# Kernel optimization log

Measured on AMD Instinct MI355X. Metric: run time of the kernel, lower is better.

The kernel has to match this reference:

```python
import jax, jax.numpy as jnp
import numpy as np

E, P, K, V, H, NE = 768, 256, 32, 32, 128, 8
B, M_DIM, T_DIM = 16, 4, 512


def setup_inputs() -> dict:
    key = jax.random.key(0)
    ks = jax.random.split(key, 24)
    s = 0.05
    inp = {
        'token_embeddings': jax.random.normal(ks[0], (B, M_DIM, T_DIM, E), jnp.float32),
        'U': jax.random.uniform(ks[1], (B, M_DIM, T_DIM), jnp.float32),
        'R': jax.random.uniform(ks[2], (B, M_DIM, M_DIM, T_DIM), jnp.float32),
        'S': jax.random.uniform(ks[3], (B, M_DIM, M_DIM, T_DIM), jnp.float32),
        'W_tp': jax.random.normal(ks[4], (E, P), jnp.float32) * s,
        'b_tp': jnp.zeros((P,), jnp.float32),
        'W_q': jax.random.normal(ks[5], (P, K), jnp.float32) * s,
        'b_q': jnp.zeros((K,), jnp.float32),
        'W_k': jax.random.normal(ks[6], (2, K), jnp.float32) * s,
        'b_k': jnp.zeros((K,), jnp.float32),
        'W_v': jax.random.normal(ks[7], (2, V), jnp.float32) * s,
        'b_v': jnp.zeros((V,), jnp.float32),
        'W_ih': jax.random.normal(ks[8], (3 * H, 1 + V), jnp.float32) * s,
        'W_hh': jax.random.normal(ks[9], (3 * H, H), jnp.float32) * s,
        'b_ih': jnp.zeros((3 * H,), jnp.float32),
        'b_hh': jnp.zeros((3 * H,), jnp.float32),
        'W1': jax.random.normal(ks[10], (P + H, (P + H) // 2), jnp.float32) * s,
        'b1': jnp.zeros(((P + H) // 2,), jnp.float32),
        'W2': jax.random.normal(ks[11], ((P + H) // 2, NE), jnp.float32) * s,
        'b2': jnp.zeros((NE,), jnp.float32),
        'M': M_DIM,
        'T': T_DIM,
    }
    return inp


def _gru(x, W_ih, W_hh, b_ih, b_hh):
    # x: [N, T, D] -> outputs [N, T, H]; PyTorch GRU cell math
    N, T, _ = x.shape
    Hh = W_hh.shape[1]
    gi = jnp.einsum('ntd,gd->ntg', x, W_ih) + b_ih  # [N,T,3H] precomputed input gates
    gi = jnp.transpose(gi, (1, 0, 2))  # [T,N,3H]

    def step(h, gi_t):
        gh = h @ W_hh.T + b_hh
        i_r, i_z, i_n = jnp.split(gi_t, 3, axis=-1)
        h_r, h_z, h_n = jnp.split(gh, 3, axis=-1)
        r = jax.nn.sigmoid(i_r + h_r)
        z = jax.nn.sigmoid(i_z + h_z)
        n = jnp.tanh(i_n + r * h_n)
        h_new = (1.0 - z) * n + z * h
        return h_new, h_new

    h0 = jnp.zeros((N, Hh), x.dtype)
    _, hs = jax.lax.scan(step, h0, gi)
    return jnp.transpose(hs, (1, 0, 2))  # [N,T,H]


def reference(token_embeddings, U, R, S, W_tp, b_tp, W_q, b_q, W_k, b_k, W_v, b_v,
              W_ih, W_hh, b_ih, b_hh, W1, b1, W2, b2, M, T):
    Bn, Mn, Tn, _ = token_embeddings.shape
    proc = jax.nn.relu(token_embeddings @ W_tp + b_tp)           # [B,M,T,P]
    query = proc @ W_q + b_q                                     # [B,M,T,K]
    Rp = jnp.transpose(R, (0, 3, 1, 2))                          # [B,T,M,M]
    Sp = jnp.transpose(S, (0, 3, 1, 2))
    pf = jnp.stack([Rp, Sp], axis=-1)                            # [B,T,M,M,2]
    keys = pf @ W_k + b_k                                        # [B,T,M,M,K]
    vals = pf @ W_v + b_v                                        # [B,T,M,M,V]
    scores = jnp.einsum('bmtk,btmjk->bmtj', query, keys) / np.sqrt(K)
    diag = jnp.eye(Mn, dtype=bool)                               # exclude j == m
    scores = jnp.where(diag[None, :, None, :], -1e9, scores)
    w = jax.nn.softmax(scores, axis=-1)                          # [B,M,T,M]
    ctx = jnp.einsum('bmtj,btmjv->bmtv', w, vals)                # [B,M,T,V]
    gru_in = jnp.concatenate([U[..., None], ctx], axis=-1)       # [B,M,T,1+V]
    gru_out = _gru(gru_in.reshape(Bn * Mn, Tn, 1 + V), W_ih, W_hh, b_ih, b_hh)
    rus_ctx = gru_out.reshape(Bn, Mn, Tn, H)
    combined = jnp.concatenate([proc, rus_ctx], axis=-1)         # [B,M,T,P+H]
    hidden = jax.nn.relu(combined @ W1 + b1)
    logits = hidden @ W2 + b2                                    # [B,M,T,NE]
    return logits
```

## Files before the change

kernel.cpp:

```cpp
#include <hip/hip_runtime.h>


typedef __attribute__((ext_vector_type(8))) short short8;
typedef __attribute__((ext_vector_type(4))) float f32x4;

__device__ __forceinline__ float bf2f(unsigned short u) {
    return __uint_as_float(((unsigned int)u) << 16);
}
__device__ __forceinline__ unsigned short f2bf(float f) {
    unsigned int x = __float_as_uint(f);
    return (unsigned short)((x + 0x7FFFu + ((x >> 16) & 1u)) >> 16);
}
__device__ __forceinline__ float sigm(float x) { return 1.0f / (1.0f + __expf(-x)); }
__device__ __forceinline__ float tanh_fast(float x) {
    x = fminf(fmaxf(x, -15.0f), 15.0f);
    float e = __expf(-2.0f * x);
    return (1.0f - e) / (1.0f + e);
}
__device__ __forceinline__ float dpp_xor1_add(float v) {
    int o = __builtin_amdgcn_update_dpp(0, __float_as_int(v), 0xB1, 0xF, 0xF, true);
    return v + __int_as_float(o);
}
__device__ __forceinline__ float sel4(f32x4 c, int sel) {
    float t0 = (sel & 1) ? c[1] : c[0];
    float t1 = (sel & 1) ? c[3] : c[2];
    return (sel & 2) ? t1 : t0;
}

#define CST_SC   768
#define CST_WU   800
#define CST_WA2  1184
#define CST_WB2  1568
#define CST_CC   1952

__global__ void k_paint(float* out, float val, int nmax) {
    int i = blockIdx.x * blockDim.x + threadIdx.x;
    if (i < nmax) out[i] = val;
}

__global__ void k_prep(const float* __restrict__ Wq,
                       const float* __restrict__ bq,
                       const float* __restrict__ Wk,
                       const float* __restrict__ bk,
                       const float* __restrict__ Wv,
                       const float* __restrict__ bv,
                       const float* __restrict__ Wih,
                       const float* __restrict__ bih,
                       float* __restrict__ cst)
{
    const int t = threadIdx.x;
    if (t < 256) {
        float a = 0.f, b = 0.f, c = 0.f;
        for (int k = 0; k < 32; ++k) {
            float w = Wq[t * 32 + k];
            a = fmaf(w, Wk[k], a);
            b = fmaf(w, Wk[32 + k], b);
            c = fmaf(w, bk[k], c);
        }
        cst[t] = a; cst[256 + t] = b; cst[512 + t] = c;
    }
    if (t == 0) {
        float ca = 0.f, cb = 0.f, cc = 0.f;
        for (int k = 0; k < 32; ++k) {
            float bqk = bq[k];
            ca = fmaf(bqk, Wk[k], ca);
            cb = fmaf(bqk, Wk[32 + k], cb);
            cc = fmaf(bqk, bk[k], cc);
        }
        cst[CST_SC + 0] = ca; cst[CST_SC + 1] = cb; cst[CST_SC + 2] = cc;
    }
    if (t < 384) {
        cst[CST_WU + t] = Wih[t * 33];
        float a2 = 0.f, b2 = 0.f, c2 = bih[t];
        for (int v = 0; v < 32; ++v) {
            float w = Wih[t * 33 + 1 + v];
            a2 = fmaf(w, Wv[v], a2);
            b2 = fmaf(w, Wv[32 + v], b2);
            c2 = fmaf(w, bv[v], c2);
        }
        cst[CST_WA2 + t] = a2; cst[CST_WB2 + t] = b2; cst[CST_CC + t] = c2;
    }
}

__global__ __launch_bounds__(256) void k_proc(
    const float* __restrict__ A,
    const float* __restrict__ Bw,
    const float* __restrict__ bias,
    unsigned short* __restrict__ C)
{
    __shared__ unsigned short A_s[128 * 40];
    __shared__ unsigned short B_s[64 * 40];
    const int t = threadIdx.x;
    const int row0 = blockIdx.y * 128;
    const int col0 = blockIdx.x * 64;
    const int lane = t & 63, wave = t >> 6;
    const int wr = wave >> 1, wc = wave & 1;
    const int quad = lane >> 4, l16 = lane & 15;

    f32x4 acc[4][2] = {};

    for (int k0 = 0; k0 < 768; k0 += 32) {
        {
            const int r = t >> 1, kq = (t & 1) * 16;
            const float* src = A + (size_t)(row0 + r) * 768 + k0 + kq;
            float4 v0 = *(const float4*)(src);
            float4 v1 = *(const float4*)(src + 4);
            float4 v2 = *(const float4*)(src + 8);
            float4 v3 = *(const float4*)(src + 12);
            short8 s0, s1;
            s0[0] = f2bf(v0.x); s0[1] = f2bf(v0.y); s0[2] = f2bf(v0.z); s0[3] = f2bf(v0.w);
            s0[4] = f2bf(v1.x); s0[5] = f2bf(v1.y); s0[6] = f2bf(v1.z); s0[7] = f2bf(v1.w);
            s1[0] = f2bf(v2.x); s1[1] = f2bf(v2.y); s1[2] = f2bf(v2.z); s1[3] = f2bf(v2.w);
            s1[4] = f2bf(v3.x); s1[5] = f2bf(v3.y); s1[6] = f2bf(v3.z); s1[7] = f2bf(v3.w);
            *(short8*)(A_s + r * 40 + kq) = s0;
            *(short8*)(A_s + r * 40 + kq + 8) = s1;
        }
        {
            const int k = t >> 3, nq = (t & 7) * 8;
            const float* src = Bw + (size_t)(k0 + k) * 256 + col0 + nq;
            float4 v0 = *(const float4*)(src);
            float4 v1 = *(const float4*)(src + 4);
            B_s[(nq + 0) * 40 + k] = f2bf(v0.x);
            B_s[(nq + 1) * 40 + k] = f2bf(v0.y);
            B_s[(nq + 2) * 40 + k] = f2bf(v0.z);
            B_s[(nq + 3) * 40 + k] = f2bf(v0.w);
            B_s[(nq + 4) * 40 + k] = f2bf(v1.x);
            B_s[(nq + 5) * 40 + k] = f2bf(v1.y);
            B_s[(nq + 6) * 40 + k] = f2bf(v1.z);
            B_s[(nq + 7) * 40 + k] = f2bf(v1.w);
        }
        __syncthreads();
        short8 af[4], bf[2];
        #pragma unroll
        for (int im = 0; im < 4; ++im)
            af[im] = *(const short8*)(A_s + (wr * 64 + im * 16 + l16) * 40 + quad * 8);
        #pragma unroll
        for (int in = 0; in < 2; ++in)
            bf[in] = *(const short8*)(B_s + (wc * 32 + in * 16 + l16) * 40 + quad * 8);
        #pragma unroll
        for (int im = 0; im < 4; ++im)
            #pragma unroll
            for (int in = 0; in < 2; ++in)
                acc[im][in] = __builtin_amdgcn_mfma_f32_16x16x32_bf16(
                    af[im], bf[in], acc[im][in], 0, 0, 0);
        __syncthreads();
    }
    float bias_v[2];
    #pragma unroll
    for (int in = 0; in < 2; ++in) bias_v[in] = bias[col0 + wc * 32 + in * 16 + l16];
    #pragma unroll
    for (int im = 0; im < 4; ++im)
        #pragma unroll
        for (int in = 0; in < 2; ++in) {
            const int c_g = col0 + wc * 32 + in * 16 + l16;
            #pragma unroll
            for (int reg = 0; reg < 4; ++reg) {
                const int r_g = row0 + wr * 64 + im * 16 + quad * 4 + reg;
                float v = fmaxf(acc[im][in][reg] + bias_v[in], 0.f);
                C[(size_t)r_g * 256 + c_g] = f2bf(v);
            }
        }
}

__global__ __launch_bounds__(256) void k_attn(
    const unsigned short* __restrict__ proc,
    const float* __restrict__ R,
    const float* __restrict__ S,
    const float* __restrict__ cst,
    float* __restrict__ wrws)
{
    __shared__ float wv_s[768];
    const int tid = threadIdx.x;
    for (int i = tid; i < 768; i += 256) wv_s[i] = cst[i];
    __syncthreads();

    const int lane = tid & 63, wave = tid >> 6;
    const int row = blockIdx.x * 4 + wave;
    const int t = row & 511, m = (row >> 9) & 3, b = row >> 11;
    const int p0 = lane * 4;

    ushort4 u = *(const ushort4*)(proc + (size_t)row * 256 + p0);
    float p0f = bf2f(u.x), p1f = bf2f(u.y), p2f = bf2f(u.z), p3f = bf2f(u.w);
    float dA = 0.f, dB = 0.f, dC = 0.f;
    dA = fmaf(p0f, wv_s[p0 + 0], dA); dB = fmaf(p0f, wv_s[256 + p0 + 0], dB); dC = fmaf(p0f, wv_s[512 + p0 + 0], dC);
    dA = fmaf(p1f, wv_s[p0 + 1], dA); dB = fmaf(p1f, wv_s[256 + p0 + 1], dB); dC = fmaf(p1f, wv_s[512 + p0 + 1], dC);
    dA = fmaf(p2f, wv_s[p0 + 2], dA); dB = fmaf(p2f, wv_s[256 + p0 + 2], dB); dC = fmaf(p2f, wv_s[512 + p0 + 2], dC);
    dA = fmaf(p3f, wv_s[p0 + 3], dA); dB = fmaf(p3f, wv_s[256 + p0 + 3], dB); dC = fmaf(p3f, wv_s[512 + p0 + 3], dC);
    #pragma unroll
    for (int mm = 1; mm < 64; mm <<= 1) {
        dA += __shfl_xor(dA, mm, 64);
        dB += __shfl_xor(dB, mm, 64);
        dC += __shfl_xor(dC, mm, 64);
    }
    if (lane == 0) {
        dA += cst[CST_SC + 0]; dB += cst[CST_SC + 1]; dC += cst[CST_SC + 2];
        const float scale = 0.17677669529663687f;
        float rr[4], ss[4], sc[4], mx = -1e30f;
        #pragma unroll
        for (int j = 0; j < 4; ++j) {
            const size_t idx = ((size_t)(b * 16 + m * 4 + j)) * 512 + t;
            rr[j] = R[idx]; ss[j] = S[idx];
            float v = (rr[j] * dA + ss[j] * dB + dC) * scale;
            if (j == m) v = -1e9f;
            sc[j] = v; mx = fmaxf(mx, v);
        }
        float w[4], se = 0.f;
        #pragma unroll
        for (int j = 0; j < 4; ++j) { w[j] = __expf(sc[j] - mx); se += w[j]; }
        const float inv = 1.0f / se;
        float wr = 0.f, wss = 0.f;
        #pragma unroll
        for (int j = 0; j < 4; ++j) { wr += w[j] * rr[j]; wss += w[j] * ss[j]; }
        float2 o; o.x = wr * inv; o.y = wss * inv;
        ((float2*)wrws)[row] = o;
    }
}

__global__ __launch_bounds__(256) void k_gru(
    const float* __restrict__ wrws,
    const float* __restrict__ U,
    const float* __restrict__ Whh,
    const float* __restrict__ bhh,
    const float* __restrict__ cst,
    unsigned short* __restrict__ gout)
{
    __shared__ unsigned short hbuf[2][2][144];
    __shared__ float4 uvw_s[512];

    const int tid  = threadIdx.x;
    const int lane = tid & 63, w = tid >> 6;
    const int l16  = lane & 15, quad = lane >> 4;
    const int n    = blockIdx.x;
    const int par  = l16 & 1;
    const int sel  = (l16 >> 1) & 3;
    const int hh   = (l16 >> 3) & 1;
    const int eg   = 32 * w + 16 * hh + quad * 4 + sel;
    const bool writer = (par == 0);

    short8 afr[3][2][4];
    #pragma unroll
    for (int g3 = 0; g3 < 3; ++g3)
        #pragma unroll
        for (int h2 = 0; h2 < 2; ++h2) {
            const int row = g3 * 128 + 32 * w + 16 * h2 + l16;
            const float* rp = Whh + (size_t)row * 128 + quad * 8;
            #pragma unroll
            for (int kf = 0; kf < 4; ++kf) {
                float4 v0 = *(const float4*)(rp + kf * 32);
                float4 v1 = *(const float4*)(rp + kf * 32 + 4);
                short8 s;
                s[0] = f2bf(v0.x); s[1] = f2bf(v0.y); s[2] = f2bf(v0.z); s[3] = f2bf(v0.w);
                s[4] = f2bf(v1.x); s[5] = f2bf(v1.y); s[6] = f2bf(v1.z); s[7] = f2bf(v1.w);
                afr[g3][h2][kf] = s;
            }
        }

    const float wu_r = cst[CST_WU  + eg], wu_z = cst[CST_WU  + 128 + eg], wu_n = cst[CST_WU  + 256 + eg];
    const float wa_r = cst[CST_WA2 + eg], wa_z = cst[CST_WA2 + 128 + eg], wa_n = cst[CST_WA2 + 256 + eg];
    const float wb_r = cst[CST_WB2 + eg], wb_z = cst[CST_WB2 + 128 + eg], wb_n = cst[CST_WB2 + 256 + eg];
    const float cc_r = cst[CST_CC  + eg] + bhh[eg];
    const float cc_z = cst[CST_CC  + 128 + eg] + bhh[128 + eg];
    const float cc_n = cst[CST_CC  + 256 + eg];
    const float bh_n = bhh[256 + eg];

    for (int i = tid; i < 512; i += 256) {
        float u = U[(size_t)n * 512 + i];
        float2 w2 = ((const float2*)wrws)[(size_t)n * 512 + i];
        float4 p; p.x = u; p.y = w2.x; p.z = w2.y; p.w = 0.f;
        uvw_s[i] = p;
    }
    for (int i = tid; i < 288; i += 256) ((unsigned int*)hbuf)[i] = 0u;
    __syncthreads();

    float h_old = 0.f;
    const f32x4 ZZ = {0.f, 0.f, 0.f, 0.f};

    #pragma unroll 2
    for (int t = 0; t < 512; ++t) {
        const int cur = t & 1, nxt = cur ^ 1;

        const unsigned short* hb = &hbuf[cur][par][0];
        short8 bfr[4];
        #pragma unroll
        for (int kf = 0; kf < 4; ++kf)
            bfr[kf] = *(const short8*)(hb + kf * 32 + quad * 8);
        const float4 uvw = uvw_s[t];

        f32x4 c[6] = {ZZ, ZZ, ZZ, ZZ, ZZ, ZZ};
        #pragma unroll
        for (int kf = 0; kf < 4; ++kf)
            #pragma unroll
            for (int j = 0; j < 6; ++j)
                c[j] = __builtin_amdgcn_mfma_f32_16x16x32_bf16(
                    afr[j >> 1][j & 1][kf], bfr[kf], c[j], 0, 0, 0);

        float gh[3];
        #pragma unroll
        for (int g3 = 0; g3 < 3; ++g3) {
            const float v0 = sel4(c[2 * g3 + 0], sel);
            const float v1 = sel4(c[2 * g3 + 1], sel);
            gh[g3] = dpp_xor1_add(hh ? v1 : v0);
        }

        const float gir = fmaf(uvw.z, wb_r, fmaf(uvw.y, wa_r, fmaf(uvw.x, wu_r, cc_r)));
        const float giz = fmaf(uvw.z, wb_z, fmaf(uvw.y, wa_z, fmaf(uvw.x, wu_z, cc_z)));
        const float gin = fmaf(uvw.z, wb_n, fmaf(uvw.y, wa_n, fmaf(uvw.x, wu_n, cc_n)));
        const float r  = sigm(gir + gh[0]);
        const float z  = sigm(giz + gh[1]);
        const float nn = tanh_fast(fmaf(r, gh[2] + bh_n, gin));
        const float hn = fmaf(z, h_old - nn, nn);
        h_old = hn;

        if (writer) {
            const unsigned short hi16 = f2bf(hn);
            hbuf[nxt][0][eg] = hi16;
            hbuf[nxt][1][eg] = f2bf(hn - bf2f(hi16));
            gout[((size_t)n * 512 + t) * 128 + eg] = hi16;
        }
        asm volatile("s_waitcnt lgkmcnt(0)" ::: "memory");
        __builtin_amdgcn_s_barrier();
        asm volatile("" ::: "memory");
        __builtin_amdgcn_sched_barrier(0x7);
    }
}

__global__ __launch_bounds__(256) void k_hid(
    const unsigned short* __restrict__ proc,
    const unsigned short* __restrict__ gout,
    const float* __restrict__ W1,
    const float* __restrict__ b1,
    const float* __restrict__ W2,
    const float* __restrict__ b2,
    float* __restrict__ out)
{
    __shared__ __align__(16) unsigned char smem[56480];
    unsigned short* As = (unsigned short*)smem;
    unsigned short* Bh = (unsigned short*)(smem + 5120);
    unsigned short* Bl = (unsigned short*)(smem + 20480);
    float* Hs  = (float*)smem;
    float* W2t = (float*)(smem + 50176);
    float* b2s = (float*)(smem + 56448);

    const int tid = threadIdx.x;
    const int row0 = blockIdx.x * 64;
    const int lane = tid & 63, w = tid >> 6;
    const int l16 = lane & 15, quad = lane >> 4;

    for (int i = tid; i < 1536; i += 256) {
        const int c = i >> 3, e = i & 7;
        W2t[e * 196 + c] = W2[i];
    }
    if (tid < 8) b2s[tid] = b2[tid];

    const int ar = tid >> 2, akq = (tid & 3) * 8;
    const int bk2 = (tid >> 4) * 2, bc0 = tid & 15;

    f32x4 acc[4][3] = {};

    for (int k0 = 0; k0 < 384; k0 += 32) {
        __syncthreads();
        {
            const int kk = k0 + akq;
            short8 v;
            if (kk < 256) v = *(const short8*)(proc + (size_t)(row0 + ar) * 256 + kk);
            else          v = *(const short8*)(gout + (size_t)(row0 + ar) * 128 + (kk - 256));
            *(short8*)(As + ar * 40 + akq) = v;
        }
        {
            const float* wrow0 = W1 + (size_t)(k0 + bk2) * 192;
            const float* wrow1 = wrow0 + 192;
            #pragma unroll
            for (int j = 0; j < 12; ++j) {
                const int c = bc0 + 16 * j;
                const float f0 = wrow0[c], f1 = wrow1[c];
                const unsigned short h0 = f2bf(f0), h1 = f2bf(f1);
                const unsigned short s0 = f2bf(f0 - bf2f(h0));
                const unsigned short s1 = f2bf(f1 - bf2f(h1));
                *(unsigned int*)(Bh + c * 40 + bk2) = (unsigned int)h0 | ((unsigned int)h1 << 16);
                *(unsigned int*)(Bl + c * 40 + bk2) = (unsigned int)s0 | ((unsigned int)s1 << 16);
            }
        }
        __syncthreads();
        short8 af[4], bh[3], bl[3];
        #pragma unroll
        for (int m = 0; m < 4; ++m)
            af[m] = *(const short8*)(As + (m * 16 + l16) * 40 + quad * 8);
        #pragma unroll
        for (int nn = 0; nn < 3; ++nn) {
            const int col = w * 48 + nn * 16 + l16;
            bh[nn] = *(const short8*)(Bh + col * 40 + quad * 8);
            bl[nn] = *(const short8*)(Bl + col * 40 + quad * 8);
        }
        #pragma unroll
        for (int m = 0; m < 4; ++m)
            #pragma unroll
            for (int nn = 0; nn < 3; ++nn) {
                acc[m][nn] = __builtin_amdgcn_mfma_f32_16x16x32_bf16(af[m], bh[nn], acc[m][nn], 0, 0, 0);
                acc[m][nn] = __builtin_amdgcn_mfma_f32_16x16x32_bf16(af[m], bl[nn], acc[m][nn], 0, 0, 0);
            }
    }
    __syncthreads();
    {
        float b1v[3];
        #pragma unroll
        for (int nn = 0; nn < 3; ++nn) b1v[nn] = b1[w * 48 + nn * 16 + l16];
        #pragma unroll
        for (int m = 0; m < 4; ++m)
            #pragma unroll
            for (int nn = 0; nn < 3; ++nn) {
                const int col = w * 48 + nn * 16 + l16;
                #pragma unroll
                for (int reg = 0; reg < 4; ++reg) {
                    const int row = m * 16 + quad * 4 + reg;
                    Hs[row * 196 + col] = fmaxf(acc[m][nn][reg] + b1v[nn], 0.f);
                }
            }
    }
    __syncthreads();
    const int r = tid >> 2, qq = tid & 3;
    const int e0 = 2 * qq, e1 = e0 + 1;
    float s0 = b2s[e0], s1 = b2s[e1];
    const float* hrow = Hs + r * 196;
    const float* w0 = W2t + e0 * 196;
    const float* w1 = W2t + e1 * 196;
    #pragma unroll 8
    for (int c = 0; c < 192; c += 4) {
        float4 h4 = *(const float4*)(hrow + c);
        float4 a4 = *(const float4*)(w0 + c);
        float4 b4 = *(const float4*)(w1 + c);
        s0 = fmaf(h4.x, a4.x, fmaf(h4.y, a4.y, fmaf(h4.z, a4.z, fmaf(h4.w, a4.w, s0))));
        s1 = fmaf(h4.x, b4.x, fmaf(h4.y, b4.y, fmaf(h4.z, b4.z, fmaf(h4.w, b4.w, s1))));
    }
    out[(size_t)(row0 + r) * 8 + e0] = s0;
    out[(size_t)(row0 + r) * 8 + e1] = s1;
}

extern "C" void kernel_launch(void* const* d_in, const int* in_sizes, int n_in,
                              void* d_out, int out_size, void* d_ws, size_t ws_size,
                              hipStream_t stream) {
    const float* emb  = (const float*)d_in[0];
    const float* U    = (const float*)d_in[1];
    const float* R    = (const float*)d_in[2];
    const float* S    = (const float*)d_in[3];
    const float* W_tp = (const float*)d_in[4];
    const float* b_tp = (const float*)d_in[5];
    const float* W_q  = (const float*)d_in[6];
    const float* b_q  = (const float*)d_in[7];
    const float* W_k  = (const float*)d_in[8];
    const float* b_k  = (const float*)d_in[9];
    const float* W_v  = (const float*)d_in[10];
    const float* b_v  = (const float*)d_in[11];
    const float* W_ih = (const float*)d_in[12];
    const float* W_hh = (const float*)d_in[13];
    const float* b_ih = (const float*)d_in[14];
    const float* b_hh = (const float*)d_in[15];
    const float* W1   = (const float*)d_in[16];
    const float* b1   = (const float*)d_in[17];
    const float* W2   = (const float*)d_in[18];
    const float* b2   = (const float*)d_in[19];

    float* outp = (float*)d_out;

    const size_t NEEDED = 25444352u;
    if (ws_size < NEEDED) {
        k_paint<<<(out_size + 255) / 256, 256, 0, stream>>>(outp, 3.0f, out_size);
        return;
    }

    char* ws = (char*)d_ws;
    unsigned short* proc = (unsigned short*)(ws);
    float*          wrws = (float*)(ws + 16777216u);
    unsigned short* gout = (unsigned short*)(ws + 17039360u);
    float*          cst  = (float*)(ws + 25427968u);

    k_prep<<<1, 512, 0, stream>>>(W_q, b_q, W_k, b_k, W_v, b_v, W_ih, b_ih, cst);
    k_proc<<<dim3(4, 256), 256, 0, stream>>>(emb, W_tp, b_tp, proc);
    k_attn<<<8192, 256, 0, stream>>>(proc, R, S, cst, wrws);
    k_gru <<<64, 256, 0, stream>>>(wrws, U, W_hh, b_hh, cst, gout);
    k_hid <<<512, 256, 0, stream>>>(proc, gout, W1, b1, W2, b2, outp);
}
```

Before: 524.8 us.

## Pre-transpose and bf16-convert GEMM weights once, load B fragments directly from global

Weight matrices W_tp and W1 are now converted to bf16 (W1 as hi/lo split) and transposed once in the prep kernel. k_proc and k_hid load B fragments straight from global memory into registers, with a one-step register prefetch, instead of having every block re-convert and scatter the weights into shared memory. This removes redundant per-block conversion work and LDS traffic. In exchange, the prep kernel becomes heavier, using 8 blocks with strided (uncoalesced) transposed writes, and B reads now depend on cache hits.

```diff
diff --git a/kernel.cpp b/kernel.cpp
--- a/kernel.cpp
+++ b/kernel.cpp
@@ -46,50 +46,68 @@
                        const float* __restrict__ bv,
                        const float* __restrict__ Wih,
                        const float* __restrict__ bih,
-                       float* __restrict__ cst)
+                       const float* __restrict__ Wtp,
+                       const float* __restrict__ W1,
+                       float* __restrict__ cst,
+                       unsigned short* __restrict__ wtpT,
+                       unsigned short* __restrict__ w1hT,
+                       unsigned short* __restrict__ w1lT)
 {
     const int t = threadIdx.x;
-    if (t < 256) {
-        float a = 0.f, b = 0.f, c = 0.f;
-        for (int k = 0; k < 32; ++k) {
-            float w = Wq[t * 32 + k];
-            a = fmaf(w, Wk[k], a);
-            b = fmaf(w, Wk[32 + k], b);
-            c = fmaf(w, bk[k], c);
-        }
-        cst[t] = a; cst[256 + t] = b; cst[512 + t] = c;
-    }
-    if (t == 0) {
-        float ca = 0.f, cb = 0.f, cc = 0.f;
-        for (int k = 0; k < 32; ++k) {
-            float bqk = bq[k];
-            ca = fmaf(bqk, Wk[k], ca);
-            cb = fmaf(bqk, Wk[32 + k], cb);
-            cc = fmaf(bqk, bk[k], cc);
-        }
-        cst[CST_SC + 0] = ca; cst[CST_SC + 1] = cb; cst[CST_SC + 2] = cc;
-    }
-    if (t < 384) {
-        cst[CST_WU + t] = Wih[t * 33];
-        float a2 = 0.f, b2 = 0.f, c2 = bih[t];
-        for (int v = 0; v < 32; ++v) {
-            float w = Wih[t * 33 + 1 + v];
-            a2 = fmaf(w, Wv[v], a2);
-            b2 = fmaf(w, Wv[32 + v], b2);
-            c2 = fmaf(w, bv[v], c2);
-        }
-        cst[CST_WA2 + t] = a2; cst[CST_WB2 + t] = b2; cst[CST_CC + t] = c2;
+    if (blockIdx.x == 0) {
+        if (t < 256) {
+            float a = 0.f, b = 0.f, c = 0.f;
+            for (int k = 0; k < 32; ++k) {
+                float w = Wq[t * 32 + k];
+                a = fmaf(w, Wk[k], a);
+                b = fmaf(w, Wk[32 + k], b);
+                c = fmaf(w, bk[k], c);
+            }
+            cst[t] = a; cst[256 + t] = b; cst[512 + t] = c;
+        }
+        if (t == 0) {
+            float ca = 0.f, cb = 0.f, cc = 0.f;
+            for (int k = 0; k < 32; ++k) {
+                float bqk = bq[k];
+                ca = fmaf(bqk, Wk[k], ca);
+                cb = fmaf(bqk, Wk[32 + k], cb);
+                cc = fmaf(bqk, bk[k], cc);
+            }
+            cst[CST_SC + 0] = ca; cst[CST_SC + 1] = cb; cst[CST_SC + 2] = cc;
+        }
+        if (t < 384) {
+            cst[CST_WU + t] = Wih[t * 33];
+            float a2 = 0.f, b2 = 0.f, c2 = bih[t];
+            for (int v = 0; v < 32; ++v) {
+                float w = Wih[t * 33 + 1 + v];
+                a2 = fmaf(w, Wv[v], a2);
+                b2 = fmaf(w, Wv[32 + v], b2);
+                c2 = fmaf(w, bv[v], c2);
+            }
+            cst[CST_WA2 + t] = a2; cst[CST_WB2 + t] = b2; cst[CST_CC + t] = c2;
+        }
+    }
+    const int gt = blockIdx.x * 512 + t;
+    for (int i = gt; i < 196608; i += 4096) {
+        const int k = i >> 8, c = i & 255;
+        wtpT[c * 768 + k] = f2bf(Wtp[i]);
+    }
+    for (int i = gt; i < 73728; i += 4096) {
+        const int k = i / 192, c = i - k * 192;
+        const float w = W1[i];
+        const unsigned short h = f2bf(w);
+        w1hT[c * 384 + k] = h;
+        w1lT[c * 384 + k] = f2bf(w - bf2f(h));
     }
 }
 
 __global__ __launch_bounds__(256) void k_proc(
     const float* __restrict__ A,
-    const float* __restrict__ Bw,
+    const unsigned short* __restrict__ BwT,
     const float* __restrict__ bias,
     unsigned short* __restrict__ C)
 {
     __shared__ unsigned short A_s[128 * 40];
-    __shared__ unsigned short B_s[64 * 40];
     const int t = threadIdx.x;
     const int row0 = blockIdx.y * 128;
     const int col0 = blockIdx.x * 64;
@@ -98,6 +116,12 @@
     const int quad = lane >> 4, l16 = lane & 15;
 
     f32x4 acc[4][2] = {};
+
+    const unsigned short* bp0 = BwT + (size_t)(col0 + wc * 32 + l16) * 768 + quad * 8;
+    const unsigned short* bp1 = bp0 + 16 * 768;
+    short8 bf_cur[2];
+    bf_cur[0] = *(const short8*)(bp0);
+    bf_cur[1] = *(const short8*)(bp1);
 
     for (int k0 = 0; k0 < 768; k0 += 32) {
         {
@@ -115,35 +139,25 @@
             *(short8*)(A_s + r * 40 + kq) = s0;
             *(short8*)(A_s + r * 40 + kq + 8) = s1;
         }
-        {
-            const int k = t >> 3, nq = (t & 7) * 8;
-            const float* src = Bw + (size_t)(k0 + k) * 256 + col0 + nq;
-            float4 v0 = *(const float4*)(src);
-            float4 v1 = *(const float4*)(src + 4);
-            B_s[(nq + 0) * 40 + k] = f2bf(v0.x);
-            B_s[(nq + 1) * 40 + k] = f2bf(v0.y);
-            B_s[(nq + 2) * 40 + k] = f2bf(v0.z);
-            B_s[(nq + 3) * 40 + k] = f2bf(v0.w);
-            B_s[(nq + 4) * 40 + k] = f2bf(v1.x);
-            B_s[(nq + 5) * 40 + k] = f2bf(v1.y);
-            B_s[(nq + 6) * 40 + k] = f2bf(v1.z);
-            B_s[(nq + 7) * 40 + k] = f2bf(v1.w);
-        }
         __syncthreads();
-        short8 af[4], bf[2];
+        const int kn = (k0 + 32 < 768) ? k0 + 32 : 0;
+        short8 bf_nxt[2];
+        bf_nxt[0] = *(const short8*)(bp0 + kn);
+        bf_nxt[1] = *(const short8*)(bp1 + kn);
+
+        short8 af[4];
         #pragma unroll
         for (int im = 0; im < 4; ++im)
             af[im] = *(const short8*)(A_s + (wr * 64 + im * 16 + l16) * 40 + quad * 8);
-        #pragma unroll
-        for (int in = 0; in < 2; ++in)
-            bf[in] = *(const short8*)(B_s + (wc * 32 + in * 16 + l16) * 40 + quad * 8);
         #pragma unroll
         for (int im = 0; im < 4; ++im)
             #pragma unroll
             for (int in = 0; in < 2; ++in)
                 acc[im][in] = __builtin_amdgcn_mfma_f32_16x16x32_bf16(
-                    af[im], bf[in], acc[im][in], 0, 0, 0);
+                    af[im], bf_cur[in], acc[im][in], 0, 0, 0);
         __syncthreads();
+        bf_cur[0] = bf_nxt[0];
+        bf_cur[1] = bf_nxt[1];
     }
     float bias_v[2];
     #pragma unroll
@@ -327,7 +341,8 @@
 __global__ __launch_bounds__(256) void k_hid(
     const unsigned short* __restrict__ proc,
     const unsigned short* __restrict__ gout,
-    const float* __restrict__ W1,
+    const unsigned short* __restrict__ w1hT,
+    const unsigned short* __restrict__ w1lT,
     const float* __restrict__ b1,
     const float* __restrict__ W2,
     const float* __restrict__ b2,
@@ -335,8 +350,6 @@
 {
     __shared__ __align__(16) unsigned char smem[56480];
     unsigned short* As = (unsigned short*)smem;
-    unsigned short* Bh = (unsigned short*)(smem + 5120);
-    unsigned short* Bl = (unsigned short*)(smem + 20480);
     float* Hs  = (float*)smem;
     float* W2t = (float*)(smem + 50176);
     float* b2s = (float*)(smem + 56448);
@@ -353,7 +366,21 @@
     if (tid < 8) b2s[tid] = b2[tid];
 
     const int ar = tid >> 2, akq = (tid & 3) * 8;
-    const int bk2 = (tid >> 4) * 2, bc0 = tid & 15;
+
+    const unsigned short* bph[3];
+    const unsigned short* bpl[3];
+    #pragma unroll
+    for (int nn = 0; nn < 3; ++nn) {
+        const size_t off = (size_t)(w * 48 + nn * 16 + l16) * 384 + quad * 8;
+        bph[nn] = w1hT + off;
+        bpl[nn] = w1lT + off;
+    }
+    short8 bh_cur[3], bl_cur[3];
+    #pragma unroll
+    for (int nn = 0; nn < 3; ++nn) {
+        bh_cur[nn] = *(const short8*)(bph[nn]);
+        bl_cur[nn] = *(const short8*)(bpl[nn]);
+    }
 
     f32x4 acc[4][3] = {};
 
@@ -366,38 +393,30 @@
             else          v = *(const short8*)(gout + (size_t)(row0 + ar) * 128 + (kk - 256));
             *(short8*)(As + ar * 40 + akq) = v;
         }
-        {
-            const float* wrow0 = W1 + (size_t)(k0 + bk2) * 192;
-            const float* wrow1 = wrow0 + 192;
-            #pragma unroll
-            for (int j = 0; j < 12; ++j) {
-                const int c = bc0 + 16 * j;
-                const float f0 = wrow0[c], f1 = wrow1[c];
-                const unsigned short h0 = f2bf(f0), h1 = f2bf(f1);
-                const unsigned short s0 = f2bf(f0 - bf2f(h0));
-                const unsigned short s1 = f2bf(f1 - bf2f(h1));
-                *(unsigned int*)(Bh + c * 40 + bk2) = (unsigned int)h0 | ((unsigned int)h1 << 16);
-                *(unsigned int*)(Bl + c * 40 + bk2) = (unsigned int)s0 | ((unsigned int)s1 << 16);
-            }
-        }
         __syncthreads();
-        short8 af[4], bh[3], bl[3];
+        const int kn = (k0 + 32 < 384) ? k0 + 32 : 0;
+        short8 bh_nxt[3], bl_nxt[3];
+        #pragma unroll
+        for (int nn = 0; nn < 3; ++nn) {
+            bh_nxt[nn] = *(const short8*)(bph[nn] + kn);
+            bl_nxt[nn] = *(const short8*)(bpl[nn] + kn);
+        }
+        short8 af[4];
         #pragma unroll
         for (int m = 0; m < 4; ++m)
             af[m] = *(const short8*)(As + (m * 16 + l16) * 40 + quad * 8);
-        #pragma unroll
-        for (int nn = 0; nn < 3; ++nn) {
-            const int col = w * 48 + nn * 16 + l16;
-            bh[nn] = *(const short8*)(Bh + col * 40 + quad * 8);
-            bl[nn] = *(const short8*)(Bl + col * 40 + quad * 8);
-        }
         #pragma unroll
         for (int m = 0; m < 4; ++m)
             #pragma unroll
             for (int nn = 0; nn < 3; ++nn) {
-                acc[m][nn] = __builtin_amdgcn_mfma_f32_16x16x32_bf16(af[m], bh[nn], acc[m][nn], 0, 0, 0);
-                acc[m][nn] = __builtin_amdgcn_mfma_f32_16x16x32_bf16(af[m], bl[nn], acc[m][nn], 0, 0, 0);
-            }
+                acc[m][nn] = __builtin_amdgcn_mfma_f32_16x16x32_bf16(af[m], bh_cur[nn], acc[m][nn], 0, 0, 0);
+                acc[m][nn] = __builtin_amdgcn_mfma_f32_16x16x32_bf16(af[m], bl_cur[nn], acc[m][nn], 0, 0, 0);
+            }
+        #pragma unroll
+        for (int nn = 0; nn < 3; ++nn) {
+            bh_cur[nn] = bh_nxt[nn];
+            bl_cur[nn] = bl_nxt[nn];
+        }
     }
     __syncthreads();
     {
@@ -461,7 +480,7 @@
 
     float* outp = (float*)d_out;
 
-    const size_t NEEDED = 25444352u;
+    const size_t NEEDED = 26125440u;
     if (ws_size < NEEDED) {
         k_paint<<<(out_size + 255) / 256, 256, 0, stream>>>(outp, 3.0f, out_size);
         return;
@@ -472,10 +491,14 @@
     float*          wrws = (float*)(ws + 16777216u);
     unsigned short* gout = (unsigned short*)(ws + 17039360u);
     float*          cst  = (float*)(ws + 25427968u);
-
-    k_prep<<<1, 512, 0, stream>>>(W_q, b_q, W_k, b_k, W_v, b_v, W_ih, b_ih, cst);
-    k_proc<<<dim3(4, 256), 256, 0, stream>>>(emb, W_tp, b_tp, proc);
+    unsigned short* wtpT = (unsigned short*)(ws + 25437312u);
+    unsigned short* w1hT = (unsigned short*)(ws + 25830528u);
+    unsigned short* w1lT = (unsigned short*)(ws + 25977984u);
+
+    k_prep<<<8, 512, 0, stream>>>(W_q, b_q, W_k, b_k, W_v, b_v, W_ih, b_ih,
+                                  W_tp, W1, cst, wtpT, w1hT, w1lT);
+    k_proc<<<dim3(4, 256), 256, 0, stream>>>(emb, wtpT, b_tp, proc);
     k_attn<<<8192, 256, 0, stream>>>(proc, R, S, cst, wrws);
     k_gru <<<64, 256, 0, stream>>>(wrws, U, W_hh, b_hh, cst, gout);
-    k_hid <<<512, 256, 0, stream>>>(proc, gout, W1, b1, W2, b2, outp);
-}
+    k_hid <<<512, 256, 0, stream>>>(proc, gout, w1hT, w1lT, b1, W2, b2, outp);
+}
```

New measurement: 571.3 us. 8.9% more time.

## Fuse attention computation into GRU kernel prologue

Applied to the files above, without the earlier changes.

Removes the separate attention kernel and computes the per-row attention-weighted R/S context inside the GRU kernel before the recurrence, writing directly into shared memory. This removes one kernel launch and the global round trip through the wrws buffer. In exchange, the projection dot products now run on only 64 blocks with per-thread serial loops over strided proc rows, reducing parallelism and coalescing for that phase.

```diff
diff --git a/kernel.cpp b/kernel.cpp
--- a/kernel.cpp
+++ b/kernel.cpp
@@ -162,63 +162,11 @@
         }
 }
 
-__global__ __launch_bounds__(256) void k_attn(
+__global__ __launch_bounds__(256) void k_gru(
     const unsigned short* __restrict__ proc,
-    const float* __restrict__ R,
-    const float* __restrict__ S,
-    const float* __restrict__ cst,
-    float* __restrict__ wrws)
-{
-    __shared__ float wv_s[768];
-    const int tid = threadIdx.x;
-    for (int i = tid; i < 768; i += 256) wv_s[i] = cst[i];
-    __syncthreads();
-
-    const int lane = tid & 63, wave = tid >> 6;
-    const int row = blockIdx.x * 4 + wave;
-    const int t = row & 511, m = (row >> 9) & 3, b = row >> 11;
-    const int p0 = lane * 4;
-
-    ushort4 u = *(const ushort4*)(proc + (size_t)row * 256 + p0);
-    float p0f = bf2f(u.x), p1f = bf2f(u.y), p2f = bf2f(u.z), p3f = bf2f(u.w);
-    float dA = 0.f, dB = 0.f, dC = 0.f;
-    dA = fmaf(p0f, wv_s[p0 + 0], dA); dB = fmaf(p0f, wv_s[256 + p0 + 0], dB); dC = fmaf(p0f, wv_s[512 + p0 + 0], dC);
-    dA = fmaf(p1f, wv_s[p0 + 1], dA); dB = fmaf(p1f, wv_s[256 + p0 + 1], dB); dC = fmaf(p1f, wv_s[512 + p0 + 1], dC);
-    dA = fmaf(p2f, wv_s[p0 + 2], dA); dB = fmaf(p2f, wv_s[256 + p0 + 2], dB); dC = fmaf(p2f, wv_s[512 + p0 + 2], dC);
-    dA = fmaf(p3f, wv_s[p0 + 3], dA); dB = fmaf(p3f, wv_s[256 + p0 + 3], dB); dC = fmaf(p3f, wv_s[512 + p0 + 3], dC);
-    #pragma unroll
-    for (int mm = 1; mm < 64; mm <<= 1) {
-        dA += __shfl_xor(dA, mm, 64);
-        dB += __shfl_xor(dB, mm, 64);
-        dC += __shfl_xor(dC, mm, 64);
-    }
-    if (lane == 0) {
-        dA += cst[CST_SC + 0]; dB += cst[CST_SC + 1]; dC += cst[CST_SC + 2];
-        const float scale = 0.17677669529663687f;
-        float rr[4], ss[4], sc[4], mx = -1e30f;
-        #pragma unroll
-        for (int j = 0; j < 4; ++j) {
-            const size_t idx = ((size_t)(b * 16 + m * 4 + j)) * 512 + t;
-            rr[j] = R[idx]; ss[j] = S[idx];
-            float v = (rr[j] * dA + ss[j] * dB + dC) * scale;
-            if (j == m) v = -1e9f;
-            sc[j] = v; mx = fmaxf(mx, v);
-        }
-        float w[4], se = 0.f;
-        #pragma unroll
-        for (int j = 0; j < 4; ++j) { w[j] = __expf(sc[j] - mx); se += w[j]; }
-        const float inv = 1.0f / se;
-        float wr = 0.f, wss = 0.f;
-        #pragma unroll
-        for (int j = 0; j < 4; ++j) { wr += w[j] * rr[j]; wss += w[j] * ss[j]; }
-        float2 o; o.x = wr * inv; o.y = wss * inv;
-        ((float2*)wrws)[row] = o;
-    }
-}
-
-__global__ __launch_bounds__(256) void k_gru(
-    const float* __restrict__ wrws,
     const float* __restrict__ U,
+    const float* __restrict__ Rg,
+    const float* __restrict__ Sg,
     const float* __restrict__ Whh,
     const float* __restrict__ bhh,
     const float* __restrict__ cst,
@@ -226,6 +174,7 @@
 {
     __shared__ unsigned short hbuf[2][2][144];
     __shared__ float4 uvw_s[512];
+    __shared__ float wv_s[768];
 
     const int tid  = threadIdx.x;
     const int lane = tid & 63, w = tid >> 6;
@@ -263,13 +212,49 @@
     const float cc_n = cst[CST_CC  + 256 + eg];
     const float bh_n = bhh[256 + eg];
 
-    for (int i = tid; i < 512; i += 256) {
-        float u = U[(size_t)n * 512 + i];
-        float2 w2 = ((const float2*)wrws)[(size_t)n * 512 + i];
-        float4 p; p.x = u; p.y = w2.x; p.z = w2.y; p.w = 0.f;
-        uvw_s[i] = p;
-    }
+    for (int i = tid; i < 768; i += 256) wv_s[i] = cst[i];
     for (int i = tid; i < 288; i += 256) ((unsigned int*)hbuf)[i] = 0u;
+    __syncthreads();
+
+    {
+        const float scA = cst[CST_SC + 0], scB = cst[CST_SC + 1], scC = cst[CST_SC + 2];
+        const int m = n & 3;
+        const float scale = 0.17677669529663687f;
+        for (int rr = tid; rr < 512; rr += 256) {
+            const unsigned short* pr = proc + ((size_t)n * 512 + rr) * 256;
+            float dA = scA, dB = scB, dC = scC;
+            for (int kk = 0; kk < 256; kk += 8) {
+                short8 v = *(const short8*)(pr + kk);
+                #pragma unroll
+                for (int e = 0; e < 8; ++e) {
+                    const float f = bf2f((unsigned short)v[e]);
+                    dA = fmaf(f, wv_s[kk + e], dA);
+                    dB = fmaf(f, wv_s[256 + kk + e], dB);
+                    dC = fmaf(f, wv_s[512 + kk + e], dC);
+                }
+            }
+            float rv[4], sv[4], sc4[4], mx = -1e30f;
+            #pragma unroll
+            for (int j = 0; j < 4; ++j) {
+                const size_t idx = ((size_t)(4 * n + j)) * 512 + rr;
+                rv[j] = Rg[idx]; sv[j] = Sg[idx];
+                float v = (rv[j] * dA + sv[j] * dB + dC) * scale;
+                if (j == m) v = -1e9f;
+                sc4[j] = v; mx = fmaxf(mx, v);
+            }
+            float wj[4], se = 0.f;
+            #pragma unroll
+            for (int j = 0; j < 4; ++j) { wj[j] = __expf(sc4[j] - mx); se += wj[j]; }
+            const float inv = 1.0f / se;
+            float wrk = 0.f, wsk = 0.f;
+            #pragma unroll
+            for (int j = 0; j < 4; ++j) { wrk += wj[j] * rv[j]; wsk += wj[j] * sv[j]; }
+            float4 p;
+            p.x = U[(size_t)n * 512 + rr];
+            p.y = wrk * inv; p.z = wsk * inv; p.w = 0.f;
+            uvw_s[rr] = p;
+        }
+    }
     __syncthreads();
 
     float h_old = 0.f;
@@ -469,13 +454,11 @@
 
     char* ws = (char*)d_ws;
     unsigned short* proc = (unsigned short*)(ws);
-    float*          wrws = (float*)(ws + 16777216u);
     unsigned short* gout = (unsigned short*)(ws + 17039360u);
     float*          cst  = (float*)(ws + 25427968u);
 
     k_prep<<<1, 512, 0, stream>>>(W_q, b_q, W_k, b_k, W_v, b_v, W_ih, b_ih, cst);
     k_proc<<<dim3(4, 256), 256, 0, stream>>>(emb, W_tp, b_tp, proc);
-    k_attn<<<8192, 256, 0, stream>>>(proc, R, S, cst, wrws);
-    k_gru <<<64, 256, 0, stream>>>(wrws, U, W_hh, b_hh, cst, gout);
+    k_gru <<<64, 256, 0, stream>>>(proc, U, R, S, W_hh, b_hh, cst, gout);
     k_hid <<<512, 256, 0, stream>>>(proc, gout, W1, b1, W2, b2, outp);
 }
```

Result: no change. 530.2 us (+1.0%).
